# Performance work log

Measured on AMD Instinct MI355X. Metric: run time of the kernel, lower is better.

Reference implementation:

```python
import jax, jax.numpy as jnp
import numpy as np

N_NODES = 50000
N_RELS = 8
IN_DIM = 128
OUT_DIM = 128
N_EDGES = 800000


def setup_inputs() -> dict:
    key = jax.random.key(0)
    k1, k2, k3, k4 = jax.random.split(key, 4)
    src = jax.random.randint(k1, (N_EDGES,), 0, N_NODES, dtype=jnp.int64 if jax.config.jax_enable_x64 else jnp.int32)
    rel = jax.random.randint(k2, (N_EDGES,), 0, N_RELS, dtype=src.dtype)
    tgt = jax.random.randint(k3, (N_EDGES,), 0, N_NODES, dtype=src.dtype)
    triples = jnp.stack([src, rel, tgt], axis=1)  # (E, 3) like torch layout (s, r, t)
    features = jax.random.normal(k4, (N_NODES, IN_DIM), dtype=jnp.float32)
    weights = jax.random.normal(jax.random.fold_in(key, 1), (N_RELS, IN_DIM, OUT_DIM), dtype=jnp.float32) * (1.0 / np.sqrt(IN_DIM))
    bias = jnp.zeros((OUT_DIM,), dtype=jnp.float32)
    return {"triples": triples, "features": features, "weights": weights, "bias": bias}


def reference(triples, features, weights, bias):
    # RGCN-NC forward, horizontal stacking (featured mode):
    #   out[t] = sum_{(s,r,t) in E} (1/c_{t,r}) * features[s] @ W[r] + bias
    # where c_{t,r} = #edges sharing the same (relation, target) pair,
    # matching sum_sparse(..., row_normalisation=False) on the (n x r*n) adjacency.
    src, rel, tgt = triples[:, 0], triples[:, 1], triples[:, 2]
    n = features.shape[0]
    r = weights.shape[0]
    e = triples.shape[0]

    # per-(rel, tgt) edge counts -> 1/c normalization per edge
    key = rel * n + tgt  # column index of horizontally stacked adjacency
    counts = jax.ops.segment_sum(jnp.ones((e,), dtype=features.dtype), key, num_segments=r * n)
    vals = 1.0 / counts[key]  # (E,)

    # dense per-relation transform: H[r] = X @ W[r]   (r, n, out)
    h = jnp.einsum('ni,rio->rno', features, weights)

    # gather per-edge messages, scale, scatter-add into targets
    msgs = h[rel, src] * vals[:, None]  # (E, out)
    out = jax.ops.segment_sum(msgs, tgt, num_segments=n)  # (n, out)
    return out + bias
```

## Files before the change

### kernel.cpp

```cpp
#include <hip/hip_runtime.h>
#include <hip/hip_bf16.h>

#define N_NODES 50000
#define N_RELS 8
#define IN_DIM 128
#define OUT_DIM 128
#define N_EDGES 800000
#define NR (N_NODES * N_RELS)
#define KDIM (N_RELS * IN_DIM)
#define SCAN_ELEMS 2048
#define SCAN_NBLK ((NR + SCAN_ELEMS - 1) / SCAN_ELEMS)
#define M_PAD 50048
#define CNT_BLKS ((N_EDGES / 4 + 255) / 256)
#define CW_BLKS ((N_RELS * IN_DIM * OUT_DIM + 255) / 256)
#define FB_BLKS ((N_NODES * IN_DIM / 8 + 255) / 256)

typedef __attribute__((ext_vector_type(8))) short bf16x8;
typedef __attribute__((ext_vector_type(4))) float floatx4;

__device__ inline unsigned short f2bf(float f) {
    unsigned u = __builtin_bit_cast(unsigned, f);
    u += 0x7fff + ((u >> 16) & 1);
    return (unsigned short)(u >> 16);
}
__device__ inline float bflo(unsigned u) {
    return __builtin_bit_cast(float, u << 16);
}
__device__ inline float bfhi(unsigned u) {
    return __builtin_bit_cast(float, u & 0xffff0000u);
}

__global__ void prep_kernel(const int* __restrict__ tri, const float* __restrict__ W,
                            const float* __restrict__ features,
                            int* __restrict__ cnt, unsigned short* __restrict__ Wtf,
                            unsigned short* __restrict__ featB) {
    const int b = blockIdx.x;
    if (b < CNT_BLKS) {
        int t = b * 256 + threadIdx.x;
        if (t >= N_EDGES / 4) return;
        const int4* tri4 = (const int4*)tri;
        int4 a = tri4[3 * t], v = tri4[3 * t + 1], c = tri4[3 * t + 2];
        atomicAdd(&cnt[a.z * N_RELS + a.y], 1);
        atomicAdd(&cnt[v.y * N_RELS + v.x], 1);
        atomicAdd(&cnt[c.x * N_RELS + v.w], 1);
        atomicAdd(&cnt[c.w * N_RELS + c.z], 1);
    } else if (b < CNT_BLKS + CW_BLKS) {
        int idx = (b - CNT_BLKS) * 256 + threadIdx.x;
        if (idx >= N_RELS * IN_DIM * OUT_DIM) return;
        int e  = idx & 7;
        int l  = (idx >> 3) & 63;
        int ks = (idx >> 9) & 31;
        int nt = idx >> 14;
        int o = nt * 16 + (l & 15);
        int k = ks * 32 + (l >> 4) * 8 + e;
        Wtf[idx] = f2bf(W[(k >> 7) * (IN_DIM * OUT_DIM) + (k & 127) * OUT_DIM + o]);
    } else {
        int t = (b - CNT_BLKS - CW_BLKS) * 256 + threadIdx.x;
        if (t >= N_NODES * IN_DIM / 8) return;
        const float4* f4 = (const float4*)features;
        float4 x = f4[2 * t], y = f4[2 * t + 1];
        uint4 o;
        o.x = (unsigned)f2bf(x.x) | ((unsigned)f2bf(x.y) << 16);
        o.y = (unsigned)f2bf(x.z) | ((unsigned)f2bf(x.w) << 16);
        o.z = (unsigned)f2bf(y.x) | ((unsigned)f2bf(y.y) << 16);
        o.w = (unsigned)f2bf(y.z) | ((unsigned)f2bf(y.w) << 16);
        ((uint4*)featB)[t] = o;
    }
}

__global__ void scan_part(const int* __restrict__ cnt, int* __restrict__ bsum) {
    __shared__ int s[256];
    int b = blockIdx.x, t = threadIdx.x;
    int base = b * SCAN_ELEMS + t * 8;
    int sum = 0;
#pragma unroll
    for (int k = 0; k < 8; ++k) {
        int i = base + k;
        sum += (i < NR) ? cnt[i] : 0;
    }
    s[t] = sum; __syncthreads();
    for (int off = 128; off > 0; off >>= 1) {
        if (t < off) s[t] += s[t + off];
        __syncthreads();
    }
    if (t == 0) bsum[b] = s[0];
}

__global__ __launch_bounds__(256) void scan_fused(
    const int* __restrict__ cnt, const int* __restrict__ bsum,
    int* __restrict__ segOff, int* __restrict__ cursor)
{
    __shared__ int s[256];
    __shared__ int sboff;
    const int b = blockIdx.x, t = threadIdx.x;

    int vb = (t < SCAN_NBLK) ? bsum[t] : 0;
    s[t] = vb; __syncthreads();
    for (int off = 1; off < 256; off <<= 1) {
        int x = (t >= off) ? s[t - off] : 0;
        __syncthreads();
        s[t] += x;
        __syncthreads();
    }
    if (t == 0) sboff = (b == 0) ? 0 : s[b - 1];
    __syncthreads();
    const int boff = sboff;

    const int base = b * SCAN_ELEMS + t * 8;
    int v[8]; int sum = 0;
#pragma unroll
    for (int k = 0; k < 8; ++k) {
        int i = base + k;
        v[k] = (i < NR) ? cnt[i] : 0;
        sum += v[k];
    }
    s[t] = sum; __syncthreads();
    for (int off = 1; off < 256; off <<= 1) {
        int x = (t >= off) ? s[t - off] : 0;
        __syncthreads();
        s[t] += x;
        __syncthreads();
    }
    int run = boff + s[t] - sum;
#pragma unroll
    for (int k = 0; k < 8; ++k) {
        int i = base + k;
        if (i < NR) { segOff[i] = run; cursor[i] = run; run += v[k]; }
    }
    if (b == 0 && t == 0) segOff[NR] = N_EDGES;
}

__global__ void scatter_kernel(const int* __restrict__ tri, int* __restrict__ cursor,
                               int* __restrict__ sortedSrc) {
    int e = blockIdx.x * 256 + threadIdx.x;
    if (e >= N_EDGES) return;
    int src = tri[3 * e];
    int rel = tri[3 * e + 1];
    int tgt = tri[3 * e + 2];
    int p = atomicAdd(&cursor[tgt * N_RELS + rel], 1);
    sortedSrc[p] = src;
}

__global__ __launch_bounds__(256) void agg_kernel(
    const int* __restrict__ sortedSrc, const int* __restrict__ segOff,
    const unsigned short* __restrict__ featB, unsigned short* __restrict__ aggG)
{
    const int wave = threadIdx.x >> 6, lane = threadIdx.x & 63;
    const int node = blockIdx.x * 4 + wave;
    const int q = lane >> 4, l16 = lane & 15;

    int bnd = 0;
    if (lane < 9) bnd = segOff[node * N_RELS + lane];
    int s[9];
#pragma unroll
    for (int i = 0; i < 9; ++i) s[i] = __shfl(bnd, i);

    const int e0 = s[0], eN = s[8];
    int srcw = 0;
    if (e0 + lane < eN) srcw = sortedSrc[e0 + lane];

    const unsigned short* fb = featB + 8 * l16;
    unsigned short* dst = aggG + (size_t)node * KDIM + 8 * l16;

#pragma unroll
    for (int p = 0; p < 2; ++p) {
        const int r = 4 * p + q;
        const int s0v = s[r], s1v = s[r + 1];
        const int len = s1v - s0v;
        int m0x = __shfl_xor(len, 16);
        int jm = (len > m0x) ? len : m0x;
        int m1x = __shfl_xor(jm, 32);
        const int jmax = (jm > m1x) ? jm : m1x;
        float a0 = 0.f, a1 = 0.f, a2 = 0.f, a3 = 0.f;
        float a4 = 0.f, a5 = 0.f, a6 = 0.f, a7 = 0.f;
        for (int j = 0; j < jmax; ++j) {
            const int e = s0v + j;
            const int i0 = e - e0;
            const int swin = __shfl(srcw, i0 & 63);
            if (j < len) {
                const int src = (i0 < 64) ? swin : sortedSrc[e];
                uint4 u = *(const uint4*)&fb[src * IN_DIM];
                a0 += bflo(u.x); a1 += bfhi(u.x);
                a2 += bflo(u.y); a3 += bfhi(u.y);
                a4 += bflo(u.z); a5 += bfhi(u.z);
                a6 += bflo(u.w); a7 += bfhi(u.w);
            }
        }
        const float inv = (len > 0) ? 1.0f / (float)len : 0.0f;
        uint4 pk;
        pk.x = (unsigned)f2bf(a0 * inv) | ((unsigned)f2bf(a1 * inv) << 16);
        pk.y = (unsigned)f2bf(a2 * inv) | ((unsigned)f2bf(a3 * inv) << 16);
        pk.z = (unsigned)f2bf(a4 * inv) | ((unsigned)f2bf(a5 * inv) << 16);
        pk.w = (unsigned)f2bf(a6 * inv) | ((unsigned)f2bf(a7 * inv) << 16);
        *(uint4*)&dst[r * IN_DIM] = pk;
    }
}

__global__ __launch_bounds__(256) void gemm_kernel(
    const unsigned short* __restrict__ aggG,
    const unsigned short* __restrict__ Wtf,
    const float* __restrict__ bias,
    float* __restrict__ out)
{
    __shared__ unsigned short Abuf[64 * 128];
    const int tid = threadIdx.x;
    const int wave = tid >> 6, lane = tid & 63;
    const int qk = lane >> 4, ln16 = lane & 15;
    const int m0 = blockIdx.x * 64;
    const int wm = wave & 1, wn = wave >> 1;

    floatx4 acc[2][4];
#pragma unroll
    for (int st = 0; st < 2; ++st)
#pragma unroll
        for (int nt = 0; nt < 4; ++nt) acc[st][nt] = (floatx4){0.f, 0.f, 0.f, 0.f};

    const int l4 = lane >> 4, l15 = lane & 15;

    for (int c = 0; c < 8; ++c) {
        __syncthreads();
#pragma unroll
        for (int i = 0; i < 4; ++i) {
            const int row = wave * 16 + i * 4 + l4;
            const int unit = l15 ^ (row & 15);
            const unsigned short* g =
                aggG + (size_t)(m0 + row) * KDIM + c * 128 + unit * 8;
            __builtin_amdgcn_global_load_lds(
                (const __attribute__((address_space(1))) unsigned int*)g,
                (__attribute__((address_space(3))) unsigned int*)&Abuf[(wave * 16 + i * 4) * 128],
                16, 0, 0);
        }
        __syncthreads();

#pragma unroll
        for (int ksl = 0; ksl < 4; ++ksl) {
            const int ks = c * 4 + ksl;
            bf16x8 a[2];
#pragma unroll
            for (int st = 0; st < 2; ++st) {
                const int r = wm * 32 + st * 16 + ln16;
                const int u = (ksl * 4 + qk) ^ (r & 15);
                a[st] = *(const bf16x8*)&Abuf[r * 128 + u * 8];
            }
#pragma unroll
            for (int nt = 0; nt < 4; ++nt) {
                const int ntg = wn * 4 + nt;
                bf16x8 b = *(const bf16x8*)&Wtf[(size_t)((ntg * 32 + ks) * 64 + lane) * 8];
                acc[0][nt] = __builtin_amdgcn_mfma_f32_16x16x32_bf16(a[0], b, acc[0][nt], 0, 0, 0);
                acc[1][nt] = __builtin_amdgcn_mfma_f32_16x16x32_bf16(a[1], b, acc[1][nt], 0, 0, 0);
            }
        }
    }

#pragma unroll
    for (int nt = 0; nt < 4; ++nt) {
        const int o = (wn * 4 + nt) * 16 + ln16;
        const float bv = bias[o];
#pragma unroll
        for (int st = 0; st < 2; ++st)
#pragma unroll
            for (int j = 0; j < 4; ++j) {
                const int t = m0 + wm * 32 + st * 16 + qk * 4 + j;
                if (t < N_NODES) out[(size_t)t * OUT_DIM + o] = acc[st][nt][j] + bv;
            }
    }
}

extern "C" void kernel_launch(void* const* d_in, const int* in_sizes, int n_in,
                              void* d_out, int out_size, void* d_ws, size_t ws_size,
                              hipStream_t stream)
{
    const int*   tri      = (const int*)d_in[0];
    const float* features = (const float*)d_in[1];
    const float* W        = (const float*)d_in[2];
    const float* bias     = (const float*)d_in[3];
    float* out = (float*)d_out;

    char* ws = (char*)d_ws;
    unsigned short* Wtf = (unsigned short*)ws; ws += (size_t)OUT_DIM * KDIM * 2;
    int* cnt       = (int*)ws; ws += (size_t)NR * 4;
    int* segOff    = (int*)ws; ws += (size_t)(NR + 4) * 4;
    int* cursor    = (int*)ws; ws += (size_t)NR * 4;
    int* bsum      = (int*)ws; ws += (size_t)SCAN_NBLK * 4;
    int* sortedSrc = (int*)ws; ws += (size_t)N_EDGES * 4;
    unsigned short* featB = (unsigned short*)ws; ws += (size_t)N_NODES * IN_DIM * 2;
    unsigned short* aggG  = (unsigned short*)ws; ws += (size_t)M_PAD * KDIM * 2;
    (void)ws_size; (void)in_sizes; (void)n_in; (void)out_size;

    hipMemsetAsync(cnt, 0, NR * sizeof(int), stream);
    prep_kernel<<<CNT_BLKS + CW_BLKS + FB_BLKS, 256, 0, stream>>>(tri, W, features, cnt, Wtf, featB);
    scan_part<<<SCAN_NBLK, 256, 0, stream>>>(cnt, bsum);
    scan_fused<<<SCAN_NBLK, 256, 0, stream>>>(cnt, bsum, segOff, cursor);
    scatter_kernel<<<(N_EDGES + 255) / 256, 256, 0, stream>>>(tri, cursor, sortedSrc);
    agg_kernel<<<N_NODES / 4, 256, 0, stream>>>(sortedSrc, segOff, featB, aggG);
    gemm_kernel<<<M_PAD / 64, 256, 0, stream>>>(aggG, Wtf, bias, out);
}
```

Measured before the change: 262.8 us.

## Fuse preprocessing, scan and scatter into one cooperative grid-synced kernel

Replaces the memset plus four preprocessing kernels (count, two-stage scan, scatter) with a single cooperative kernel of 1024 blocks that uses grid.sync between phases. The aim is to remove per-launch overhead and inter-kernel gaps. In exchange it relies on grid-wide barriers and a fixed grid size that may underuse the GPU in phases such as the scan, which only uses a subset of the blocks. The old multi-kernel path is kept as a fallback if the cooperative launch fails.

```diff
diff --git a/kernel.cpp b/kernel.cpp
--- a/kernel.cpp
+++ b/kernel.cpp
@@ -1,5 +1,8 @@
 #include <hip/hip_runtime.h>
 #include <hip/hip_bf16.h>
+#include <hip/hip_cooperative_groups.h>
+
+namespace cg = cooperative_groups;
 
 #define N_NODES 50000
 #define N_RELS 8
@@ -14,6 +17,8 @@
 #define CNT_BLKS ((N_EDGES / 4 + 255) / 256)
 #define CW_BLKS ((N_RELS * IN_DIM * OUT_DIM + 255) / 256)
 #define FB_BLKS ((N_NODES * IN_DIM / 8 + 255) / 256)
+#define COOP_BLOCKS 1024
+#define COOP_THREADS (COOP_BLOCKS * 256)
 
 typedef __attribute__((ext_vector_type(8))) short bf16x8;
 typedef __attribute__((ext_vector_type(4))) float floatx4;
@@ -28,6 +33,117 @@
 }
 __device__ inline float bfhi(unsigned u) {
     return __builtin_bit_cast(float, u & 0xffff0000u);
+}
+
+__global__ __launch_bounds__(256) void pipe_kernel(
+    const int* __restrict__ tri, const float* __restrict__ W,
+    const float* __restrict__ features,
+    int* __restrict__ cnt, unsigned short* __restrict__ Wtf,
+    unsigned short* __restrict__ featB,
+    int* __restrict__ bsum, int* __restrict__ segOff, int* __restrict__ cursor,
+    int* __restrict__ sortedSrc)
+{
+    cg::grid_group grid = cg::this_grid();
+    __shared__ int s[256];
+    __shared__ int sboff;
+    const int gtid = blockIdx.x * 256 + threadIdx.x;
+
+    for (int i = gtid; i < NR; i += COOP_THREADS) cnt[i] = 0;
+    for (int idx = gtid; idx < N_RELS * IN_DIM * OUT_DIM; idx += COOP_THREADS) {
+        int e  = idx & 7;
+        int l  = (idx >> 3) & 63;
+        int ks = (idx >> 9) & 31;
+        int nt = idx >> 14;
+        int o = nt * 16 + (l & 15);
+        int k = ks * 32 + (l >> 4) * 8 + e;
+        Wtf[idx] = f2bf(W[(k >> 7) * (IN_DIM * OUT_DIM) + (k & 127) * OUT_DIM + o]);
+    }
+    for (int t = gtid; t < N_NODES * IN_DIM / 8; t += COOP_THREADS) {
+        const float4* f4 = (const float4*)features;
+        float4 x = f4[2 * t], y = f4[2 * t + 1];
+        uint4 o;
+        o.x = (unsigned)f2bf(x.x) | ((unsigned)f2bf(x.y) << 16);
+        o.y = (unsigned)f2bf(x.z) | ((unsigned)f2bf(x.w) << 16);
+        o.z = (unsigned)f2bf(y.x) | ((unsigned)f2bf(y.y) << 16);
+        o.w = (unsigned)f2bf(y.z) | ((unsigned)f2bf(y.w) << 16);
+        ((uint4*)featB)[t] = o;
+    }
+    grid.sync();
+
+    for (int t = gtid; t < N_EDGES / 4; t += COOP_THREADS) {
+        const int4* tri4 = (const int4*)tri;
+        int4 a = tri4[3 * t], v = tri4[3 * t + 1], c = tri4[3 * t + 2];
+        atomicAdd(&cnt[a.z * N_RELS + a.y], 1);
+        atomicAdd(&cnt[v.y * N_RELS + v.x], 1);
+        atomicAdd(&cnt[c.x * N_RELS + v.w], 1);
+        atomicAdd(&cnt[c.w * N_RELS + c.z], 1);
+    }
+    grid.sync();
+
+    if (blockIdx.x < SCAN_NBLK) {
+        const int b = blockIdx.x, t = threadIdx.x;
+        const int base = b * SCAN_ELEMS + t * 8;
+        int sum = 0;
+#pragma unroll
+        for (int k = 0; k < 8; ++k) {
+            int i = base + k;
+            sum += (i < NR) ? cnt[i] : 0;
+        }
+        s[t] = sum; __syncthreads();
+        for (int off = 128; off > 0; off >>= 1) {
+            if (t < off) s[t] += s[t + off];
+            __syncthreads();
+        }
+        if (t == 0) bsum[b] = s[0];
+    }
+    grid.sync();
+
+    if (blockIdx.x < SCAN_NBLK) {
+        const int b = blockIdx.x, t = threadIdx.x;
+        int vb = (t < SCAN_NBLK) ? bsum[t] : 0;
+        s[t] = vb; __syncthreads();
+        for (int off = 1; off < 256; off <<= 1) {
+            int x = (t >= off) ? s[t - off] : 0;
+            __syncthreads();
+            s[t] += x;
+            __syncthreads();
+        }
+        if (t == 0) sboff = (b == 0) ? 0 : s[b - 1];
+        __syncthreads();
+        const int boff = sboff;
+
+        const int base = b * SCAN_ELEMS + t * 8;
+        int v[8]; int sum = 0;
+#pragma unroll
+        for (int k = 0; k < 8; ++k) {
+            int i = base + k;
+            v[k] = (i < NR) ? cnt[i] : 0;
+            sum += v[k];
+        }
+        s[t] = sum; __syncthreads();
+        for (int off = 1; off < 256; off <<= 1) {
+            int x = (t >= off) ? s[t - off] : 0;
+            __syncthreads();
+            s[t] += x;
+            __syncthreads();
+        }
+        int run = boff + s[t] - sum;
+#pragma unroll
+        for (int k = 0; k < 8; ++k) {
+            int i = base + k;
+            if (i < NR) { segOff[i] = run; cursor[i] = run; run += v[k]; }
+        }
+        if (b == 0 && t == 0) segOff[NR] = N_EDGES;
+    }
+    grid.sync();
+
+    for (int e = gtid; e < N_EDGES; e += COOP_THREADS) {
+        int src = tri[3 * e];
+        int rel = tri[3 * e + 1];
+        int tgt = tri[3 * e + 2];
+        int p = atomicAdd(&cursor[tgt * N_RELS + rel], 1);
+        sortedSrc[p] = src;
+    }
 }
 
 __global__ void prep_kernel(const int* __restrict__ tri, const float* __restrict__ W,
@@ -287,11 +403,20 @@
     unsigned short* aggG  = (unsigned short*)ws; ws += (size_t)M_PAD * KDIM * 2;
     (void)ws_size; (void)in_sizes; (void)n_in; (void)out_size;
 
-    hipMemsetAsync(cnt, 0, NR * sizeof(int), stream);
-    prep_kernel<<<CNT_BLKS + CW_BLKS + FB_BLKS, 256, 0, stream>>>(tri, W, features, cnt, Wtf, featB);
-    scan_part<<<SCAN_NBLK, 256, 0, stream>>>(cnt, bsum);
-    scan_fused<<<SCAN_NBLK, 256, 0, stream>>>(cnt, bsum, segOff, cursor);
-    scatter_kernel<<<(N_EDGES + 255) / 256, 256, 0, stream>>>(tri, cursor, sortedSrc);
+    void* args[10] = { (void*)&tri, (void*)&W, (void*)&features, (void*)&cnt,
+                       (void*)&Wtf, (void*)&featB, (void*)&bsum, (void*)&segOff,
+                       (void*)&cursor, (void*)&sortedSrc };
+    hipError_t cerr = hipLaunchCooperativeKernel((const void*)pipe_kernel,
+                                                 dim3(COOP_BLOCKS), dim3(256),
+                                                 args, 0, stream);
+    if (cerr != hipSuccess) {
+        hipMemsetAsync(cnt, 0, NR * sizeof(int), stream);
+        prep_kernel<<<CNT_BLKS + CW_BLKS + FB_BLKS, 256, 0, stream>>>(tri, W, features, cnt, Wtf, featB);
+        scan_part<<<SCAN_NBLK, 256, 0, stream>>>(cnt, bsum);
+        scan_fused<<<SCAN_NBLK, 256, 0, stream>>>(cnt, bsum, segOff, cursor);
+        scatter_kernel<<<(N_EDGES + 255) / 256, 256, 0, stream>>>(tri, cursor, sortedSrc);
+    }
+
     agg_kernel<<<N_NODES / 4, 256, 0, stream>>>(sortedSrc, segOff, featB, aggG);
     gemm_kernel<<<M_PAD / 64, 256, 0, stream>>>(aggG, Wtf, bias, out);
 }
```

After: 688.0 us. +161.8%, slower.
